# Kernel optimization log

Hardware: AMD Instinct MI355X
Metric: run time of the kernel (lower is better)

The kernel has to match this reference:

```python
import jax, jax.numpy as jnp
import numpy as np


def setup_inputs() -> dict:
    key = jax.random.key(0)
    k1, k2, k3 = jax.random.split(key, 3)
    B, C, H, W = 64, 512, 28, 28
    K = 32
    std = 1.0 / (K * C) ** 0.5
    x = jax.random.normal(k1, (B, C, H, W), dtype=jnp.float32)
    codewords = jax.random.uniform(k2, (K, C), dtype=jnp.float32, minval=-std, maxval=std)
    scale = jax.random.uniform(k3, (K,), dtype=jnp.float32, minval=-1.0, maxval=0.0)
    return {"x": x, "codewords": codewords, "scale": scale}


def reference(x, codewords, scale):
    # x: (B, C, H, W) -> descriptors (B, N, C)
    B, C, H, W = x.shape
    K = codewords.shape[0]
    xd = x.reshape(B, C, H * W).transpose(0, 2, 1)  # (B, N, C)

    # scaled L2: scale_k * ||x_n - c_k||^2, expanded without (B,N,K,C) intermediate
    x_sq = jnp.sum(xd * xd, axis=-1, keepdims=True)            # (B, N, 1)
    c_sq = jnp.sum(codewords * codewords, axis=-1)             # (K,)
    xc = jnp.einsum("bnc,kc->bnk", xd, codewords)              # (B, N, K)
    dist = scale * (x_sq - 2.0 * xc + c_sq)                    # (B, N, K)

    A = jax.nn.softmax(dist, axis=2)                           # (B, N, K)

    # encoded_k = sum_n A[b,n,k] * (x[b,n] - c[k])
    wx = jnp.einsum("bnk,bnc->bkc", A, xd)                     # (B, K, C)
    wsum = jnp.sum(A, axis=1)                                  # (B, K)
    encoded = wx - wsum[:, :, None] * codewords[None, :, :]    # (B, K, C)
    return encoded
```

## Files before the change

kernel.cpp:

```cpp
#include <hip/hip_runtime.h>
#include <hip/hip_bf16.h>

#define BB 64
#define CC 512
#define NPIX 784
#define KK 32
#define NSPL 7
#define PXB 112
#define CW_S 520
#define XA_S 136

typedef __attribute__((ext_vector_type(8))) short short8;
typedef __attribute__((ext_vector_type(4))) float floatx4;
typedef __attribute__((ext_vector_type(4))) unsigned short ushort4v;

#define OFF_WP 0
#define OFF_WS (NSPL*BB*KK*CC)

__device__ __forceinline__ unsigned short f2bf(float f) {
    union { float f; unsigned u; } v; v.f = f;
    return (unsigned short)((v.u + 0x7FFFu + ((v.u >> 16) & 1u)) >> 16);
}
__device__ __forceinline__ float bf2f(unsigned short h) {
    union { unsigned u; float f; } v; v.u = ((unsigned)h) << 16; return v.f;
}

__global__ __launch_bounds__(256) void k_fused(const float* __restrict__ x,
                                               const float* __restrict__ cw,
                                               const float* __restrict__ scale,
                                               float* __restrict__ ws)
{
    __shared__ __align__(16) unsigned char u8[128 * XA_S * 2];
    __shared__ __align__(16) unsigned short A_l[KK * XA_S];
    __shared__ float csq_p[8][KK];
    __shared__ float csq_l[KK];
    __shared__ float wred[KK][8];

    unsigned short* cs = (unsigned short*)u8;
    unsigned short* xs = (unsigned short*)u8;

    const int t     = threadIdx.x;
    const int lane  = t & 63;
    const int w     = t >> 6;
    const int col   = lane & 15;
    const int quad  = lane >> 4;
    const int split = blockIdx.x;
    const int b     = blockIdx.y;
    const int p0    = split * PXB;

#pragma unroll 4
    for (int j = 0; j < 16; ++j) {
        const int qidx = t + j * 256;
        const int row = qidx >> 7, qc = qidx & 127;
        const float4 v = *(const float4*)&cw[row * CC + qc * 4];
        ushort4v p; p.x = f2bf(v.x); p.y = f2bf(v.y); p.z = f2bf(v.z); p.w = f2bf(v.w);
        *(ushort4v*)&cs[row * CW_S + qc * 4] = p;
    }
    __syncthreads();
    {
        const int k = t & 31, part = t >> 5;
        float s = 0.f;
        for (int i = 0; i < 64; ++i) {
            const float v = bf2f(cs[k * CW_S + part * 64 + i]);
            s += v * v;
        }
        csq_p[part][k] = s;
    }
    __syncthreads();
    if (t < KK) {
        float s = 0.f;
#pragma unroll
        for (int p = 0; p < 8; ++p) s += csq_p[p][t];
        csq_l[t] = s;
    }
    __syncthreads();

    const float s0 = scale[col], s1 = scale[col + 16];
    const float q0 = csq_l[col], q1 = csq_l[col + 16];

    for (int pt = w; pt < NSPL; pt += 4) {
        const int px = p0 + pt * 16 + col;
        const float* xb = x + (size_t)b * CC * NPIX + px;

        floatx4 acc0 = {0.f, 0.f, 0.f, 0.f};
        floatx4 acc1 = {0.f, 0.f, 0.f, 0.f};
        float xsqp = 0.f;
        float va[8], vb[8];

#pragma unroll
        for (int j = 0; j < 8; ++j) va[j] = xb[(size_t)(quad * 8 + j) * NPIX];

#pragma unroll
        for (int kc = 0; kc < 16; kc += 2) {
            {
                const int cb = (kc + 1) * 32 + quad * 8;
#pragma unroll
                for (int j = 0; j < 8; ++j) vb[j] = xb[(size_t)(cb + j) * NPIX];
            }
            {
#pragma unroll
                for (int j = 0; j < 8; ++j) xsqp += va[j] * va[j];
                short8 a;
#pragma unroll
                for (int j = 0; j < 8; ++j) a[j] = (short)f2bf(va[j]);
                const int cb0 = kc * 32 + quad * 8;
                const short8 b0 = *(const short8*)&cs[col * CW_S + cb0];
                const short8 b1 = *(const short8*)&cs[(col + 16) * CW_S + cb0];
                acc0 = __builtin_amdgcn_mfma_f32_16x16x32_bf16(a, b0, acc0, 0, 0, 0);
                acc1 = __builtin_amdgcn_mfma_f32_16x16x32_bf16(a, b1, acc1, 0, 0, 0);
            }
            if (kc + 2 < 16) {
                const int cb = (kc + 2) * 32 + quad * 8;
#pragma unroll
                for (int j = 0; j < 8; ++j) va[j] = xb[(size_t)(cb + j) * NPIX];
            }
            {
#pragma unroll
                for (int j = 0; j < 8; ++j) xsqp += vb[j] * vb[j];
                short8 a;
#pragma unroll
                for (int j = 0; j < 8; ++j) a[j] = (short)f2bf(vb[j]);
                const int cb1 = (kc + 1) * 32 + quad * 8;
                const short8 b0 = *(const short8*)&cs[col * CW_S + cb1];
                const short8 b1 = *(const short8*)&cs[(col + 16) * CW_S + cb1];
                acc0 = __builtin_amdgcn_mfma_f32_16x16x32_bf16(a, b0, acc0, 0, 0, 0);
                acc1 = __builtin_amdgcn_mfma_f32_16x16x32_bf16(a, b1, acc1, 0, 0, 0);
            }
        }

        xsqp += __shfl_xor(xsqp, 16);
        xsqp += __shfl_xor(xsqp, 32);

#pragma unroll
        for (int r = 0; r < 4; ++r) {
            const float xq = __shfl(xsqp, quad * 4 + r);
            const float d0 = s0 * (xq + q0 - 2.f * acc0[r]);
            const float d1 = s1 * (xq + q1 - 2.f * acc1[r]);
            float mx = fmaxf(d0, d1);
            mx = fmaxf(mx, __shfl_xor(mx, 1));
            mx = fmaxf(mx, __shfl_xor(mx, 2));
            mx = fmaxf(mx, __shfl_xor(mx, 4));
            mx = fmaxf(mx, __shfl_xor(mx, 8));
            const float e0 = __expf(d0 - mx), e1 = __expf(d1 - mx);
            float sm = e0 + e1;
            sm += __shfl_xor(sm, 1);
            sm += __shfl_xor(sm, 2);
            sm += __shfl_xor(sm, 4);
            sm += __shfl_xor(sm, 8);
            const float inv = 1.f / sm;
            const int pxl = pt * 16 + quad * 4 + r;
            A_l[col * XA_S + pxl]        = f2bf(e0 * inv);
            A_l[(col + 16) * XA_S + pxl] = f2bf(e1 * inv);
        }
    }
    __syncthreads();

    {
        const int k = t >> 3, part = t & 7;
        float s = 0.f;
#pragma unroll 7
        for (int i = 0; i < 14; ++i) s += bf2f(A_l[k * XA_S + part * 14 + i]);
        wred[k][part] = s;
    }
    {
        const ushort4v z = {0, 0, 0, 0};
        if (t < 128) *(ushort4v*)&A_l[(t >> 2) * XA_S + PXB + (t & 3) * 4] = z;
#pragma unroll
        for (int jj = 0; jj < 2; ++jj) {
            const int q = t + jj * 256;
            *(ushort4v*)&xs[(q >> 2) * XA_S + PXB + (q & 3) * 4] = z;
        }
    }
    __syncthreads();

    if (t < KK) {
        float s = 0.f;
#pragma unroll
        for (int p = 0; p < 8; ++p) s += wred[t][p];
        ws[OFF_WS + (size_t)(split * BB + b) * KK + t] = s;
    }

    const float* xbase = x + (size_t)b * CC * NPIX + p0;
    float* Wp = ws + OFF_WP;

    for (int cch = 0; cch < 4; ++cch) {
#pragma unroll 2
        for (int j = 0; j < 14; ++j) {
            const int q = t + j * 256;
            const int row = q / 28, pq = q - row * 28;
            const float4 v = *(const float4*)&xbase[(size_t)(cch * 128 + row) * NPIX + pq * 4];
            ushort4v p; p.x = f2bf(v.x); p.y = f2bf(v.y); p.z = f2bf(v.z); p.w = f2bf(v.w);
            *(ushort4v*)&xs[row * XA_S + pq * 4] = p;
        }
        __syncthreads();

        floatx4 a00 = {0.f,0.f,0.f,0.f}, a01 = {0.f,0.f,0.f,0.f};
        floatx4 a10 = {0.f,0.f,0.f,0.f}, a11 = {0.f,0.f,0.f,0.f};
#pragma unroll
        for (int ks = 0; ks < 4; ++ks) {
            const int off = ks * 32 + quad * 8;
            const short8 av0 = *(const short8*)&A_l[col * XA_S + off];
            const short8 av1 = *(const short8*)&A_l[(col + 16) * XA_S + off];
            const short8 bv0 = *(const short8*)&xs[(w * 32 + col) * XA_S + off];
            const short8 bv1 = *(const short8*)&xs[(w * 32 + 16 + col) * XA_S + off];
            a00 = __builtin_amdgcn_mfma_f32_16x16x32_bf16(av0, bv0, a00, 0, 0, 0);
            a10 = __builtin_amdgcn_mfma_f32_16x16x32_bf16(av1, bv0, a10, 0, 0, 0);
            a01 = __builtin_amdgcn_mfma_f32_16x16x32_bf16(av0, bv1, a01, 0, 0, 0);
            a11 = __builtin_amdgcn_mfma_f32_16x16x32_bf16(av1, bv1, a11, 0, 0, 0);
        }

        const size_t sb = (size_t)(split * BB + b) * KK;
        const int cb = cch * 128 + w * 32;
#pragma unroll
        for (int r = 0; r < 4; ++r) {
            const int k0 = quad * 4 + r;
            Wp[(sb + k0) * CC + cb + col]           = a00[r];
            Wp[(sb + k0) * CC + cb + 16 + col]      = a01[r];
            Wp[(sb + k0 + 16) * CC + cb + col]      = a10[r];
            Wp[(sb + k0 + 16) * CC + cb + 16 + col] = a11[r];
        }
        __syncthreads();
    }
}

__global__ __launch_bounds__(256) void k3(const float* __restrict__ cw,
                                          const float* __restrict__ ws,
                                          float* __restrict__ out)
{
    const int idx = blockIdx.x * 256 + threadIdx.x;
    const int c4 = idx & 127;
    const int k  = (idx >> 7) & 31;
    const int b  = idx >> 12;

    const float* Wp = ws + OFF_WP;
    float4 s = make_float4(0.f, 0.f, 0.f, 0.f);
#pragma unroll
    for (int sp = 0; sp < NSPL; ++sp) {
        const float4 v = *(const float4*)&Wp[((size_t)(sp * BB + b) * KK + k) * CC + c4 * 4];
        s.x += v.x; s.y += v.y; s.z += v.z; s.w += v.w;
    }
    float wsum = 0.f;
#pragma unroll
    for (int sp = 0; sp < NSPL; ++sp) wsum += ws[OFF_WS + (size_t)(sp * BB + b) * KK + k];

    const float4 c4f = *(const float4*)&cw[k * CC + c4 * 4];
    float4 o;
    o.x = s.x - wsum * c4f.x;
    o.y = s.y - wsum * c4f.y;
    o.z = s.z - wsum * c4f.z;
    o.w = s.w - wsum * c4f.w;
    *(float4*)&out[(size_t)idx * 4] = o;
}

extern "C" void kernel_launch(void* const* d_in, const int* in_sizes, int n_in,
                              void* d_out, int out_size, void* d_ws, size_t ws_size,
                              hipStream_t stream) {
    const float* x     = (const float*)d_in[0];
    const float* cw    = (const float*)d_in[1];
    const float* scale = (const float*)d_in[2];
    float* out = (float*)d_out;
    float* ws  = (float*)d_ws;

    k_fused<<<dim3(NSPL, BB), dim3(256), 0, stream>>>(x, cw, scale, ws);
    k3<<<dim3(BB * KK * CC / 4 / 256), dim3(256), 0, stream>>>(cw, ws, out);
}
```

Before: 185.7 us.

## Split into assignment kernel and aggregation kernel with bf16 A in global memory

Replaces the fused per-pixel-split kernel plus reduction kernel with two kernels. The first computes soft-assignments per 16-pixel tile, splitting the channel dimension across 4 waves and reducing through shared memory, then writes A as bf16 to a padded global buffer. The second computes A·x per 64-channel chunk over all pixels directly from global memory, folds in wsum and the codeword subtraction, and writes the output. This removes the large fp32 partial-sum buffer (7 splits × B×K×C) and its reduction pass. In exchange, x is read twice and the second kernel's strided global loads get no shared-memory staging.

Result: slower. 221.2 us (+19.1%).

```diff
diff --git a/kernel.cpp b/kernel.cpp
--- a/kernel.cpp
+++ b/kernel.cpp
@@ -1,71 +1,79 @@
 #include <hip/hip_runtime.h>
-#include <hip/hip_bf16.h>
 
 #define BB 64
 #define CC 512
 #define NPIX 784
 #define KK 32
-#define NSPL 7
-#define PXB 112
-#define CW_S 520
-#define XA_S 136
+#define NSA 49
+#define AS 800
+#define NSTEP 24
 
 typedef __attribute__((ext_vector_type(8))) short short8;
 typedef __attribute__((ext_vector_type(4))) float floatx4;
-typedef __attribute__((ext_vector_type(4))) unsigned short ushort4v;
-
-#define OFF_WP 0
-#define OFF_WS (NSPL*BB*KK*CC)
 
 __device__ __forceinline__ unsigned short f2bf(float f) {
     union { float f; unsigned u; } v; v.f = f;
     return (unsigned short)((v.u + 0x7FFFu + ((v.u >> 16) & 1u)) >> 16);
 }
-__device__ __forceinline__ float bf2f(unsigned short h) {
-    union { unsigned u; float f; } v; v.u = ((unsigned)h) << 16; return v.f;
-}
-
-__global__ __launch_bounds__(256) void k_fused(const float* __restrict__ x,
-                                               const float* __restrict__ cw,
-                                               const float* __restrict__ scale,
-                                               float* __restrict__ ws)
+__device__ __forceinline__ short8 pack8(const float4& a, const float4& b) {
+    short8 r;
+    r[0] = (short)f2bf(a.x); r[1] = (short)f2bf(a.y);
+    r[2] = (short)f2bf(a.z); r[3] = (short)f2bf(a.w);
+    r[4] = (short)f2bf(b.x); r[5] = (short)f2bf(b.y);
+    r[6] = (short)f2bf(b.z); r[7] = (short)f2bf(b.w);
+    return r;
+}
+
+__global__ __launch_bounds__(256) void kA(const float* __restrict__ x,
+                                          const float* __restrict__ cw,
+                                          const float* __restrict__ scale,
+                                          unsigned short* __restrict__ Ag)
 {
-    __shared__ __align__(16) unsigned char u8[128 * XA_S * 2];
-    __shared__ __align__(16) unsigned short A_l[KK * XA_S];
+    __shared__ __align__(16) float red[4][64][12];
     __shared__ float csq_p[8][KK];
     __shared__ float csq_l[KK];
-    __shared__ float wred[KK][8];
-
-    unsigned short* cs = (unsigned short*)u8;
-    unsigned short* xs = (unsigned short*)u8;
-
-    const int t     = threadIdx.x;
-    const int lane  = t & 63;
-    const int w     = t >> 6;
-    const int col   = lane & 15;
-    const int quad  = lane >> 4;
-    const int split = blockIdx.x;
-    const int b     = blockIdx.y;
-    const int p0    = split * PXB;
-
-#pragma unroll 4
-    for (int j = 0; j < 16; ++j) {
-        const int qidx = t + j * 256;
-        const int row = qidx >> 7, qc = qidx & 127;
-        const float4 v = *(const float4*)&cw[row * CC + qc * 4];
-        ushort4v p; p.x = f2bf(v.x); p.y = f2bf(v.y); p.z = f2bf(v.z); p.w = f2bf(v.w);
-        *(ushort4v*)&cs[row * CW_S + qc * 4] = p;
-    }
-    __syncthreads();
+
+    const int t    = threadIdx.x;
+    const int lane = t & 63, w = t >> 6;
+    const int col  = lane & 15, quad = lane >> 4;
+    const int split = blockIdx.x, b = blockIdx.y;
+    const int p0    = split * 16;
+
     {
         const int k = t & 31, part = t >> 5;
-        float s = 0.f;
-        for (int i = 0; i < 64; ++i) {
-            const float v = bf2f(cs[k * CW_S + part * 64 + i]);
-            s += v * v;
+        const float* cp = cw + k * CC + part * 64;
+        float s = 0.f;
+#pragma unroll
+        for (int i = 0; i < 16; ++i) {
+            const float4 v = *(const float4*)&cp[i * 4];
+            s += v.x * v.x + v.y * v.y + v.z * v.z + v.w * v.w;
         }
         csq_p[part][k] = s;
     }
+
+    const float* xb = x + (size_t)b * CC * NPIX + p0 + col;
+    floatx4 acc0 = {0.f, 0.f, 0.f, 0.f};
+    floatx4 acc1 = {0.f, 0.f, 0.f, 0.f};
+    float xsqp = 0.f;
+#pragma unroll
+    for (int i = 0; i < 4; ++i) {
+        const int c0 = (w * 4 + i) * 32 + quad * 8;
+        float va[8];
+#pragma unroll
+        for (int j = 0; j < 8; ++j) va[j] = xb[(size_t)(c0 + j) * NPIX];
+        const float4 c0a = *(const float4*)&cw[col * CC + c0];
+        const float4 c0b = *(const float4*)&cw[col * CC + c0 + 4];
+        const float4 c1a = *(const float4*)&cw[(col + 16) * CC + c0];
+        const float4 c1b = *(const float4*)&cw[(col + 16) * CC + c0 + 4];
+        short8 a;
+#pragma unroll
+        for (int j = 0; j < 8; ++j) { xsqp += va[j] * va[j]; a[j] = (short)f2bf(va[j]); }
+        acc0 = __builtin_amdgcn_mfma_f32_16x16x32_bf16(a, pack8(c0a, c0b), acc0, 0, 0, 0);
+        acc1 = __builtin_amdgcn_mfma_f32_16x16x32_bf16(a, pack8(c1a, c1b), acc1, 0, 0, 0);
+    }
+    *(floatx4*)&red[w][lane][0] = acc0;
+    *(floatx4*)&red[w][lane][4] = acc1;
+    red[w][lane][8] = xsqp;
     __syncthreads();
     if (t < KK) {
         float s = 0.f;
@@ -75,67 +83,26 @@
     }
     __syncthreads();
 
-    const float s0 = scale[col], s1 = scale[col + 16];
-    const float q0 = csq_l[col], q1 = csq_l[col + 16];
-
-    for (int pt = w; pt < NSPL; pt += 4) {
-        const int px = p0 + pt * 16 + col;
-        const float* xb = x + (size_t)b * CC * NPIX + px;
-
-        floatx4 acc0 = {0.f, 0.f, 0.f, 0.f};
-        floatx4 acc1 = {0.f, 0.f, 0.f, 0.f};
-        float xsqp = 0.f;
-        float va[8], vb[8];
-
-#pragma unroll
-        for (int j = 0; j < 8; ++j) va[j] = xb[(size_t)(quad * 8 + j) * NPIX];
-
-#pragma unroll
-        for (int kc = 0; kc < 16; kc += 2) {
-            {
-                const int cb = (kc + 1) * 32 + quad * 8;
-#pragma unroll
-                for (int j = 0; j < 8; ++j) vb[j] = xb[(size_t)(cb + j) * NPIX];
-            }
-            {
-#pragma unroll
-                for (int j = 0; j < 8; ++j) xsqp += va[j] * va[j];
-                short8 a;
-#pragma unroll
-                for (int j = 0; j < 8; ++j) a[j] = (short)f2bf(va[j]);
-                const int cb0 = kc * 32 + quad * 8;
-                const short8 b0 = *(const short8*)&cs[col * CW_S + cb0];
-                const short8 b1 = *(const short8*)&cs[(col + 16) * CW_S + cb0];
-                acc0 = __builtin_amdgcn_mfma_f32_16x16x32_bf16(a, b0, acc0, 0, 0, 0);
-                acc1 = __builtin_amdgcn_mfma_f32_16x16x32_bf16(a, b1, acc1, 0, 0, 0);
-            }
-            if (kc + 2 < 16) {
-                const int cb = (kc + 2) * 32 + quad * 8;
-#pragma unroll
-                for (int j = 0; j < 8; ++j) va[j] = xb[(size_t)(cb + j) * NPIX];
-            }
-            {
-#pragma unroll
-                for (int j = 0; j < 8; ++j) xsqp += vb[j] * vb[j];
-                short8 a;
-#pragma unroll
-                for (int j = 0; j < 8; ++j) a[j] = (short)f2bf(vb[j]);
-                const int cb1 = (kc + 1) * 32 + quad * 8;
-                const short8 b0 = *(const short8*)&cs[col * CW_S + cb1];
-                const short8 b1 = *(const short8*)&cs[(col + 16) * CW_S + cb1];
-                acc0 = __builtin_amdgcn_mfma_f32_16x16x32_bf16(a, b0, acc0, 0, 0, 0);
-                acc1 = __builtin_amdgcn_mfma_f32_16x16x32_bf16(a, b1, acc1, 0, 0, 0);
-            }
-        }
-
-        xsqp += __shfl_xor(xsqp, 16);
-        xsqp += __shfl_xor(xsqp, 32);
-
+    if (w == 0) {
+        floatx4 A0 = *(const floatx4*)&red[0][lane][0];
+        floatx4 A1 = *(const floatx4*)&red[0][lane][4];
+        float xq = red[0][lane][8];
+#pragma unroll
+        for (int wv = 1; wv < 4; ++wv) {
+            A0 += *(const floatx4*)&red[wv][lane][0];
+            A1 += *(const floatx4*)&red[wv][lane][4];
+            xq += red[wv][lane][8];
+        }
+        xq += __shfl_xor(xq, 16);
+        xq += __shfl_xor(xq, 32);
+        const float s0 = scale[col], s1 = scale[col + 16];
+        const float q0 = csq_l[col], q1 = csq_l[col + 16];
+        unsigned short* Ab = Ag + (size_t)b * KK * AS + p0;
 #pragma unroll
         for (int r = 0; r < 4; ++r) {
-            const float xq = __shfl(xsqp, quad * 4 + r);
-            const float d0 = s0 * (xq + q0 - 2.f * acc0[r]);
-            const float d1 = s1 * (xq + q1 - 2.f * acc1[r]);
+            const float xqr = __shfl(xq, quad * 4 + r);
+            const float d0 = s0 * (xqr + q0 - 2.f * A0[r]);
+            const float d1 = s1 * (xqr + q1 - 2.f * A1[r]);
             float mx = fmaxf(d0, d1);
             mx = fmaxf(mx, __shfl_xor(mx, 1));
             mx = fmaxf(mx, __shfl_xor(mx, 2));
@@ -148,108 +115,96 @@
             sm += __shfl_xor(sm, 4);
             sm += __shfl_xor(sm, 8);
             const float inv = 1.f / sm;
-            const int pxl = pt * 16 + quad * 4 + r;
-            A_l[col * XA_S + pxl]        = f2bf(e0 * inv);
-            A_l[(col + 16) * XA_S + pxl] = f2bf(e1 * inv);
-        }
-    }
-    __syncthreads();
-
-    {
-        const int k = t >> 3, part = t & 7;
-        float s = 0.f;
-#pragma unroll 7
-        for (int i = 0; i < 14; ++i) s += bf2f(A_l[k * XA_S + part * 14 + i]);
-        wred[k][part] = s;
-    }
-    {
-        const ushort4v z = {0, 0, 0, 0};
-        if (t < 128) *(ushort4v*)&A_l[(t >> 2) * XA_S + PXB + (t & 3) * 4] = z;
-#pragma unroll
-        for (int jj = 0; jj < 2; ++jj) {
-            const int q = t + jj * 256;
-            *(ushort4v*)&xs[(q >> 2) * XA_S + PXB + (q & 3) * 4] = z;
-        }
-    }
-    __syncthreads();
-
-    if (t < KK) {
-        float s = 0.f;
-#pragma unroll
-        for (int p = 0; p < 8; ++p) s += wred[t][p];
-        ws[OFF_WS + (size_t)(split * BB + b) * KK + t] = s;
-    }
-
-    const float* xbase = x + (size_t)b * CC * NPIX + p0;
-    float* Wp = ws + OFF_WP;
-
-    for (int cch = 0; cch < 4; ++cch) {
-#pragma unroll 2
-        for (int j = 0; j < 14; ++j) {
-            const int q = t + j * 256;
-            const int row = q / 28, pq = q - row * 28;
-            const float4 v = *(const float4*)&xbase[(size_t)(cch * 128 + row) * NPIX + pq * 4];
-            ushort4v p; p.x = f2bf(v.x); p.y = f2bf(v.y); p.z = f2bf(v.z); p.w = f2bf(v.w);
-            *(ushort4v*)&xs[row * XA_S + pq * 4] = p;
-        }
-        __syncthreads();
-
-        floatx4 a00 = {0.f,0.f,0.f,0.f}, a01 = {0.f,0.f,0.f,0.f};
-        floatx4 a10 = {0.f,0.f,0.f,0.f}, a11 = {0.f,0.f,0.f,0.f};
-#pragma unroll
-        for (int ks = 0; ks < 4; ++ks) {
-            const int off = ks * 32 + quad * 8;
-            const short8 av0 = *(const short8*)&A_l[col * XA_S + off];
-            const short8 av1 = *(const short8*)&A_l[(col + 16) * XA_S + off];
-            const short8 bv0 = *(const short8*)&xs[(w * 32 + col) * XA_S + off];
-            const short8 bv1 = *(const short8*)&xs[(w * 32 + 16 + col) * XA_S + off];
-            a00 = __builtin_amdgcn_mfma_f32_16x16x32_bf16(av0, bv0, a00, 0, 0, 0);
-            a10 = __builtin_amdgcn_mfma_f32_16x16x32_bf16(av1, bv0, a10, 0, 0, 0);
-            a01 = __builtin_amdgcn_mfma_f32_16x16x32_bf16(av0, bv1, a01, 0, 0, 0);
-            a11 = __builtin_amdgcn_mfma_f32_16x16x32_bf16(av1, bv1, a11, 0, 0, 0);
-        }
-
-        const size_t sb = (size_t)(split * BB + b) * KK;
-        const int cb = cch * 128 + w * 32;
-#pragma unroll
-        for (int r = 0; r < 4; ++r) {
-            const int k0 = quad * 4 + r;
-            Wp[(sb + k0) * CC + cb + col]           = a00[r];
-            Wp[(sb + k0) * CC + cb + 16 + col]      = a01[r];
-            Wp[(sb + k0 + 16) * CC + cb + col]      = a10[r];
-            Wp[(sb + k0 + 16) * CC + cb + 16 + col] = a11[r];
-        }
-        __syncthreads();
-    }
-}
-
-__global__ __launch_bounds__(256) void k3(const float* __restrict__ cw,
-                                          const float* __restrict__ ws,
+            Ab[col * AS + quad * 4 + r]        = f2bf(e0 * inv);
+            Ab[(col + 16) * AS + quad * 4 + r] = f2bf(e1 * inv);
+        }
+    } else if (w == 1 && split == NSA - 1) {
+        const short8 z = {0, 0, 0, 0, 0, 0, 0, 0};
+        const int k = lane >> 1, off = (lane & 1) * 8;
+        *(short8*)&Ag[(size_t)b * KK * AS + (size_t)k * AS + NPIX + off] = z;
+    }
+}
+
+__global__ __launch_bounds__(256) void kB(const float* __restrict__ x,
+                                          const float* __restrict__ cw,
+                                          const unsigned short* __restrict__ Ag,
                                           float* __restrict__ out)
 {
-    const int idx = blockIdx.x * 256 + threadIdx.x;
-    const int c4 = idx & 127;
-    const int k  = (idx >> 7) & 31;
-    const int b  = idx >> 12;
-
-    const float* Wp = ws + OFF_WP;
-    float4 s = make_float4(0.f, 0.f, 0.f, 0.f);
-#pragma unroll
-    for (int sp = 0; sp < NSPL; ++sp) {
-        const float4 v = *(const float4*)&Wp[((size_t)(sp * BB + b) * KK + k) * CC + c4 * 4];
-        s.x += v.x; s.y += v.y; s.z += v.z; s.w += v.w;
-    }
-    float wsum = 0.f;
-#pragma unroll
-    for (int sp = 0; sp < NSPL; ++sp) wsum += ws[OFF_WS + (size_t)(sp * BB + b) * KK + k];
-
-    const float4 c4f = *(const float4*)&cw[k * CC + c4 * 4];
-    float4 o;
-    o.x = s.x - wsum * c4f.x;
-    o.y = s.y - wsum * c4f.y;
-    o.z = s.z - wsum * c4f.z;
-    o.w = s.w - wsum * c4f.w;
-    *(float4*)&out[(size_t)idx * 4] = o;
+    __shared__ float wred[KK][8];
+    __shared__ float wsum_l[KK];
+
+    const int t    = threadIdx.x;
+    const int lane = t & 63, w = t >> 6;
+    const int col  = lane & 15, quad = lane >> 4;
+    const int cch  = blockIdx.x, b = blockIdx.y;
+
+    const unsigned short* Ab = Ag + (size_t)b * KK * AS;
+
+    {
+        const int k = t & 31, part = t >> 5;
+        const unsigned* ap = (const unsigned*)(Ab + (size_t)k * AS) + part * 49;
+        float s = 0.f;
+#pragma unroll
+        for (int i = 0; i < 49; ++i) {
+            const unsigned u = ap[i];
+            union { unsigned uu; float f; } lo, hi;
+            lo.uu = u << 16; hi.uu = u & 0xffff0000u;
+            s += lo.f + hi.f;
+        }
+        wred[k][part] = s;
+    }
+
+    const int c = cch * 64 + w * 16 + col;
+    const float* xp = x + ((size_t)b * CC + c) * NPIX;
+    const unsigned short* a0p = Ab + (size_t)col * AS;
+    const unsigned short* a1p = Ab + (size_t)(col + 16) * AS;
+    const int qo = quad * 8;
+
+    floatx4 acc0 = {0.f, 0.f, 0.f, 0.f};
+    floatx4 acc1 = {0.f, 0.f, 0.f, 0.f};
+#pragma unroll 6
+    for (int s = 0; s < NSTEP; ++s) {
+        const int off = s * 32 + qo;
+        const short8 av0 = *(const short8*)&a0p[off];
+        const short8 av1 = *(const short8*)&a1p[off];
+        const float4 xv0 = *(const float4*)&xp[off];
+        const float4 xv1 = *(const float4*)&xp[off + 4];
+        const short8 bv = pack8(xv0, xv1);
+        acc0 = __builtin_amdgcn_mfma_f32_16x16x32_bf16(av0, bv, acc0, 0, 0, 0);
+        acc1 = __builtin_amdgcn_mfma_f32_16x16x32_bf16(av1, bv, acc1, 0, 0, 0);
+    }
+    {
+        const int off = NSTEP * 32 + qo;
+        const short8 av0 = *(const short8*)&a0p[off];
+        const short8 av1 = *(const short8*)&a1p[off];
+        float4 xv0 = make_float4(0.f, 0.f, 0.f, 0.f);
+        float4 xv1 = make_float4(0.f, 0.f, 0.f, 0.f);
+        if (quad < 2) {
+            xv0 = *(const float4*)&xp[off];
+            xv1 = *(const float4*)&xp[off + 4];
+        }
+        const short8 bv = pack8(xv0, xv1);
+        acc0 = __builtin_amdgcn_mfma_f32_16x16x32_bf16(av0, bv, acc0, 0, 0, 0);
+        acc1 = __builtin_amdgcn_mfma_f32_16x16x32_bf16(av1, bv, acc1, 0, 0, 0);
+    }
+
+    __syncthreads();
+    if (t < KK) {
+        float s = 0.f;
+#pragma unroll
+        for (int p = 0; p < 8; ++p) s += wred[t][p];
+        wsum_l[t] = s;
+    }
+    __syncthreads();
+
+    float* ob = out + (size_t)b * KK * CC + c;
+    const float* cp = cw + c;
+#pragma unroll
+    for (int r = 0; r < 4; ++r) {
+        const int k0 = quad * 4 + r;
+        ob[(size_t)k0 * CC]        = acc0[r] - wsum_l[k0]      * cp[(size_t)k0 * CC];
+        ob[(size_t)(k0 + 16) * CC] = acc1[r] - wsum_l[k0 + 16] * cp[(size_t)(k0 + 16) * CC];
+    }
 }
 
 extern "C" void kernel_launch(void* const* d_in, const int* in_sizes, int n_in,
@@ -259,8 +214,8 @@
     const float* cw    = (const float*)d_in[1];
     const float* scale = (const float*)d_in[2];
     float* out = (float*)d_out;
-    float* ws  = (float*)d_ws;
-
-    k_fused<<<dim3(NSPL, BB), dim3(256), 0, stream>>>(x, cw, scale, ws);
-    k3<<<dim3(BB * KK * CC / 4 / 256), dim3(256), 0, stream>>>(cw, ws, out);
-}
+    unsigned short* Ag = (unsigned short*)d_ws;
+
+    kA<<<dim3(NSA, BB), dim3(256), 0, stream>>>(x, cw, scale, Ag);
+    kB<<<dim3(8, BB), dim3(256), 0, stream>>>(x, cw, Ag, out);
+}
```
